# Kernel tuning notes

Measured on AMD Instinct MI355X. Metric: run time of the kernel, lower is better.

Reference implementation:

```python
import jax, jax.numpy as jnp
import numpy as np

B, S, DIM, H, HD, K, DEPTH = 2, 2048, 1024, 16, 64, 64, 8
SCALE = 1.0 / np.sqrt(HD)


def _build_cantor_routes(seq_len: int, k: int, depth: int) -> np.ndarray:
    # Vectorized version of CantorAttention._build_cantor_routes
    pos = np.arange(seq_len, dtype=np.float64)
    x = pos / max(1, seq_len - 1)
    x = np.clip(x, 1e-06, 1.0 - 1e-06)
    cantor = np.zeros(seq_len, dtype=np.float64)
    factor = 0.5
    for _ in range(depth):
        x = x * 3.0
        digit = np.floor(x)
        x = x - digit
        cantor += factor * (digit == 2.0)
        factor *= 0.5
    cantor = cantor.astype(np.float32)
    # k nearest positions in Cantor space for each position
    dist = np.abs(cantor[:, None] - cantor[None, :])  # [S, S]
    routes = np.argsort(dist, axis=1, kind='stable')[:, :k]  # [S, k]
    return routes.astype(np.int32)


def setup_inputs() -> dict:
    key = jax.random.key(0)
    k1, k2, k3, k4, k5 = jax.random.split(key, 5)
    s = 1.0 / np.sqrt(DIM)
    return {
        'x': jax.random.normal(k1, (B, S, DIM), dtype=jnp.float32),
        'w_qkv': jax.random.normal(k2, (3 * DIM, DIM), dtype=jnp.float32) * s,
        'b_qkv': jax.random.normal(k3, (3 * DIM,), dtype=jnp.float32) * 0.01,
        'w_out': jax.random.normal(k4, (DIM, DIM), dtype=jnp.float32) * s,
        'b_out': jax.random.normal(k5, (DIM,), dtype=jnp.float32) * 0.01,
        'routes': jnp.asarray(_build_cantor_routes(S, K, DEPTH)),
    }


def reference(x, w_qkv, b_qkv, w_out, b_out, routes):
    b, s, _ = x.shape
    # QKV projection (torch Linear: y = x @ W.T + b)
    qkv = x @ w_qkv.T + b_qkv                       # [B, S, 3*DIM]
    qkv = qkv.reshape(b, s, 3, H, HD).transpose(2, 0, 3, 1, 4)  # [3, B, H, S, HD]
    q, k, v = qkv[0], qkv[1], qkv[2]                # each [B, H, S, HD]
    # Gather k/v at Cantor neighbor routes: [B, H, S, K, HD]
    k_g = jnp.take(k, routes, axis=2)
    v_g = jnp.take(v, routes, axis=2)
    scores = jnp.einsum('bhqd,bhqkd->bhqk', q, k_g) * SCALE
    attn = jax.nn.softmax(scores, axis=-1)
    out = jnp.einsum('bhqk,bhqkd->bhqd', attn, v_g)  # [B, H, S, HD]
    out = out.transpose(0, 2, 1, 3).reshape(b, s, DIM)
    return out @ w_out.T + b_out
```

## Files before the change

kernel.cpp:

```cpp
#include <hip/hip_runtime.h>

#define BQ   2
#define SQ   2048
#define DIMQ 1024
#define HQ   16
#define HDQ  64
#define KQ   64
#define QKV_STRIDE (3 * DIMQ)

typedef __attribute__((ext_vector_type(8))) short short8;
typedef __attribute__((ext_vector_type(4))) float floatx4;

typedef const __attribute__((address_space(1))) unsigned short* gas_t;
typedef __attribute__((address_space(3))) unsigned short* las_t;

__device__ __forceinline__ unsigned short f2b(float f) {
    union { float f; unsigned int u; } x; x.f = f;
    unsigned int r = x.u + 0x7fffu + ((x.u >> 16) & 1u);
    return (unsigned short)(r >> 16);
}
__device__ __forceinline__ float b2f(unsigned short u) {
    union { unsigned int u; float f; } x; x.u = ((unsigned int)u) << 16;
    return x.f;
}

__global__ __launch_bounds__(256) void cast_f32_bf16(const float* __restrict__ in,
                                                     unsigned short* __restrict__ out,
                                                     int n4) {
    int i = blockIdx.x * blockDim.x + threadIdx.x;
    if (i >= n4) return;
    float4 v = ((const float4*)in)[i];
    ushort4 o;
    o.x = f2b(v.x); o.y = f2b(v.y); o.z = f2b(v.z); o.w = f2b(v.w);
    ((ushort4*)out)[i] = o;
}

template <typename CT>
__global__ __launch_bounds__(256) void gemm_bf16_nt(const unsigned short* __restrict__ A,
                                                    const unsigned short* __restrict__ B,
                                                    const float* __restrict__ bias,
                                                    CT* __restrict__ C,
                                                    int M, int N, int K) {
    __shared__ unsigned short As[128 * 32];
    __shared__ unsigned short Bs[128 * 32];

    const int tid  = threadIdx.x;
    const int lane = tid & 63;
    const int wv   = tid >> 6;
    const int wm   = (wv >> 1) * 64;
    const int wn   = (wv & 1) * 64;
    const int fr   = lane & 15;
    const int fq   = lane >> 4;

    const int m0 = blockIdx.y * 128;
    const int n0 = blockIdx.x * 128;

    floatx4 acc[4][4];
#pragma unroll
    for (int i = 0; i < 4; ++i)
#pragma unroll
        for (int j = 0; j < 4; ++j) acc[i][j] = (floatx4)(0.f);

    const unsigned short* Ab = A + (size_t)m0 * K;
    const unsigned short* Bb = B + (size_t)n0 * K;

    for (int k0 = 0; k0 < K; k0 += 32) {
#pragma unroll
        for (int iss = 0; iss < 2; ++iss) {
            const int c   = iss * 256 + wv * 64 + lane;
            const int row = c >> 2;
            const int kc  = (c & 3) << 3;
            const int ldsbase = (iss * 256 + wv * 64) * 8;
            __builtin_amdgcn_global_load_lds(
                (gas_t)(Ab + (size_t)row * K + k0 + kc), (las_t)&As[ldsbase], 16, 0, 0);
            __builtin_amdgcn_global_load_lds(
                (gas_t)(Bb + (size_t)row * K + k0 + kc), (las_t)&Bs[ldsbase], 16, 0, 0);
        }
        __syncthreads();

        short8 af[4], bf[4];
#pragma unroll
        for (int i = 0; i < 4; ++i)
            af[i] = *(const short8*)&As[(wm + i * 16 + fr) * 32 + fq * 8];
#pragma unroll
        for (int j = 0; j < 4; ++j)
            bf[j] = *(const short8*)&Bs[(wn + j * 16 + fr) * 32 + fq * 8];
#pragma unroll
        for (int i = 0; i < 4; ++i)
#pragma unroll
            for (int j = 0; j < 4; ++j)
                acc[i][j] = __builtin_amdgcn_mfma_f32_16x16x32_bf16(af[i], bf[j], acc[i][j], 0, 0, 0);
        __syncthreads();
    }

    float bv[4];
#pragma unroll
    for (int j = 0; j < 4; ++j) bv[j] = bias[n0 + wn + j * 16 + fr];
#pragma unroll
    for (int i = 0; i < 4; ++i) {
#pragma unroll
        for (int r = 0; r < 4; ++r) {
            const size_t row = (size_t)(m0 + wm + i * 16 + fq * 4 + r);
#pragma unroll
            for (int j = 0; j < 4; ++j) {
                const float v = acc[i][j][r] + bv[j];
                if constexpr (sizeof(CT) == 2)
                    C[row * N + n0 + wn + j * 16 + fr] = (CT)f2b(v);
                else
                    C[row * N + n0 + wn + j * 16 + fr] = (CT)v;
            }
        }
    }
}

__global__ __launch_bounds__(256) void attn_kernel(const unsigned short* __restrict__ qkv,
                                                   const int* __restrict__ routes,
                                                   unsigned short* __restrict__ out) {
    __shared__ float s_s[HQ][KQ + 1];
    __shared__ int   r_s[KQ];
    __shared__ float o_part[8][132];

    const int t  = threadIdx.x;
    const int id = blockIdx.x;
    const int bq = (id & 7) * 512 + (id >> 3);
    const int b  = bq >> 11;
    const int q  = bq & 2047;

    if (t < KQ) r_s[t] = routes[q * KQ + t];

    const int g    = t >> 7;
    const int th   = t & 127;
    const int h    = th >> 3;
    const int d0   = (t & 7) * 8;

    float qf[8];
    {
        const short8 q8 = *(const short8*)&qkv[((size_t)bq * 3) * DIMQ + h * HDQ + d0];
#pragma unroll
        for (int e = 0; e < 8; ++e) qf[e] = b2f((unsigned short)q8[e]);
    }
    __syncthreads();

    const size_t baseK = ((size_t)b * SQ * 3 + 1) * DIMQ + h * HDQ + d0;
    const size_t baseV = ((size_t)b * SQ * 3 + 2) * DIMQ + h * HDQ + d0;

#pragma unroll 8
    for (int jj = 0; jj < KQ / 2; ++jj) {
        const int j = jj * 2 + g;
        const int r = r_s[j];
        const short8 k8 = *(const short8*)&qkv[baseK + (size_t)r * QKV_STRIDE];
        float p = 0.f;
#pragma unroll
        for (int e = 0; e < 8; ++e) p += qf[e] * b2f((unsigned short)k8[e]);
        p += __shfl_xor(p, 1, 64);
        p += __shfl_xor(p, 2, 64);
        p += __shfl_xor(p, 4, 64);
        if ((t & 7) == 0) s_s[h][j] = p * 0.125f;
    }
    __syncthreads();

    {
        const int lane = t & 63;
        const int sh   = ((t >> 6) << 2) + (lane >> 4);
        const int i    = lane & 15;
        float v0 = s_s[sh][i], v1 = s_s[sh][i + 16], v2 = s_s[sh][i + 32], v3 = s_s[sh][i + 48];
        float mx = fmaxf(fmaxf(v0, v1), fmaxf(v2, v3));
        mx = fmaxf(mx, __shfl_xor(mx, 1, 64));
        mx = fmaxf(mx, __shfl_xor(mx, 2, 64));
        mx = fmaxf(mx, __shfl_xor(mx, 4, 64));
        mx = fmaxf(mx, __shfl_xor(mx, 8, 64));
        float e0 = __expf(v0 - mx), e1 = __expf(v1 - mx);
        float e2 = __expf(v2 - mx), e3 = __expf(v3 - mx);
        float sm = e0 + e1 + e2 + e3;
        sm += __shfl_xor(sm, 1, 64);
        sm += __shfl_xor(sm, 2, 64);
        sm += __shfl_xor(sm, 4, 64);
        sm += __shfl_xor(sm, 8, 64);
        const float inv = 1.0f / sm;
        s_s[sh][i]      = e0 * inv;
        s_s[sh][i + 16] = e1 * inv;
        s_s[sh][i + 32] = e2 * inv;
        s_s[sh][i + 48] = e3 * inv;
    }
    __syncthreads();

    float o[8];
#pragma unroll
    for (int e = 0; e < 8; ++e) o[e] = 0.f;
#pragma unroll 8
    for (int jj = 0; jj < KQ / 2; ++jj) {
        const int   j = jj * 2 + g;
        const int   r = r_s[j];
        const float w = s_s[h][j];
        const short8 v8 = *(const short8*)&qkv[baseV + (size_t)r * QKV_STRIDE];
#pragma unroll
        for (int e = 0; e < 8; ++e) o[e] += w * b2f((unsigned short)v8[e]);
    }
    if (g == 1) {
#pragma unroll
        for (int e = 0; e < 8; ++e) o_part[e][th] = o[e];
    }
    __syncthreads();
    if (g == 0) {
        ushort4 lo, hi;
        lo.x = f2b(o[0] + o_part[0][th]); lo.y = f2b(o[1] + o_part[1][th]);
        lo.z = f2b(o[2] + o_part[2][th]); lo.w = f2b(o[3] + o_part[3][th]);
        hi.x = f2b(o[4] + o_part[4][th]); hi.y = f2b(o[5] + o_part[5][th]);
        hi.z = f2b(o[6] + o_part[6][th]); hi.w = f2b(o[7] + o_part[7][th]);
        ushort4* dst = (ushort4*)&out[(size_t)bq * DIMQ + h * HDQ + d0];
        dst[0] = lo; dst[1] = hi;
    }
}

extern "C" void kernel_launch(void* const* d_in, const int* in_sizes, int n_in,
                              void* d_out, int out_size, void* d_ws, size_t ws_size,
                              hipStream_t stream) {
    const float* x      = (const float*)d_in[0];
    const float* w_qkv  = (const float*)d_in[1];
    const float* b_qkv  = (const float*)d_in[2];
    const float* w_out  = (const float*)d_in[3];
    const float* b_out  = (const float*)d_in[4];
    const int*   routes = (const int*)d_in[5];
    float* out = (float*)d_out;

    char* ws = (char*)d_ws;
    unsigned short* qkvb  = (unsigned short*)ws;
    unsigned short* xb    = (unsigned short*)(ws + 25165824);
    unsigned short* attnb = xb;
    unsigned short* wqb   = (unsigned short*)(ws + 33554432);
    unsigned short* wob   = (unsigned short*)(ws + 39845888);

    const int M = BQ * SQ;
    dim3 blk(256);

    cast_f32_bf16<<<(M * DIMQ / 4 + 255) / 256, blk, 0, stream>>>(x, xb, M * DIMQ / 4);
    cast_f32_bf16<<<(3 * DIMQ * DIMQ / 4 + 255) / 256, blk, 0, stream>>>(w_qkv, wqb, 3 * DIMQ * DIMQ / 4);
    cast_f32_bf16<<<(DIMQ * DIMQ / 4 + 255) / 256, blk, 0, stream>>>(w_out, wob, DIMQ * DIMQ / 4);

    gemm_bf16_nt<unsigned short><<<dim3(3 * DIMQ / 128, M / 128), blk, 0, stream>>>(
        xb, wqb, b_qkv, qkvb, M, 3 * DIMQ, DIMQ);

    attn_kernel<<<BQ * SQ, blk, 0, stream>>>(qkvb, routes, attnb);

    gemm_bf16_nt<float><<<dim3(DIMQ / 128, M / 128), blk, 0, stream>>>(
        attnb, wob, b_out, out, M, DIMQ, DIMQ);
}
```

Before: 207.5 us.

## Fuse casts, add online-softmax attention, and use narrower tiles for output GEMM

The three f32-to-bf16 cast launches become one kernel that dispatches on index range, removing two launches. The attention kernel now uses an online softmax. K and V gathers are issued together in a single pass, and the two half-groups' partial results are merged with max/sum rescaling. This drops the shared score buffer, two barriers and a second gather loop. The GEMM is templated on tile sizes, and the output projection uses 128x64 tiles to double its block count for better CU fill, at the cost of more extra exp work per key and less reuse per tile.

```diff
diff --git a/kernel.cpp b/kernel.cpp
--- a/kernel.cpp
+++ b/kernel.cpp
@@ -24,85 +24,94 @@
     return x.f;
 }
 
-__global__ __launch_bounds__(256) void cast_f32_bf16(const float* __restrict__ in,
-                                                     unsigned short* __restrict__ out,
-                                                     int n4) {
+__global__ __launch_bounds__(256) void cast3_f32_bf16(const float* __restrict__ s0, unsigned short* __restrict__ d0, int n0,
+                                                      const float* __restrict__ s1, unsigned short* __restrict__ d1, int n1,
+                                                      const float* __restrict__ s2, unsigned short* __restrict__ d2, int n2) {
     int i = blockIdx.x * blockDim.x + threadIdx.x;
-    if (i >= n4) return;
-    float4 v = ((const float4*)in)[i];
+    const float* s; unsigned short* d;
+    if (i < n0)                { s = s0; d = d0; }
+    else if (i < n0 + n1)      { s = s1; d = d1; i -= n0; }
+    else if (i < n0 + n1 + n2) { s = s2; d = d2; i -= n0 + n1; }
+    else return;
+    float4 v = ((const float4*)s)[i];
     ushort4 o;
     o.x = f2b(v.x); o.y = f2b(v.y); o.z = f2b(v.z); o.w = f2b(v.w);
-    ((ushort4*)out)[i] = o;
-}
-
-template <typename CT>
+    ((ushort4*)d)[i] = o;
+}
+
+template <int BM, int BN, typename CT>
 __global__ __launch_bounds__(256) void gemm_bf16_nt(const unsigned short* __restrict__ A,
                                                     const unsigned short* __restrict__ B,
                                                     const float* __restrict__ bias,
                                                     CT* __restrict__ C,
                                                     int M, int N, int K) {
-    __shared__ unsigned short As[128 * 32];
-    __shared__ unsigned short Bs[128 * 32];
+    constexpr int MI = BM / 32;
+    constexpr int NJ = BN / 32;
+    __shared__ unsigned short As[BM * 32];
+    __shared__ unsigned short Bs[BN * 32];
 
     const int tid  = threadIdx.x;
     const int lane = tid & 63;
     const int wv   = tid >> 6;
-    const int wm   = (wv >> 1) * 64;
-    const int wn   = (wv & 1) * 64;
+    const int wm   = (wv >> 1) * (BM / 2);
+    const int wn   = (wv & 1) * (BN / 2);
     const int fr   = lane & 15;
     const int fq   = lane >> 4;
 
-    const int m0 = blockIdx.y * 128;
-    const int n0 = blockIdx.x * 128;
-
-    floatx4 acc[4][4];
-#pragma unroll
-    for (int i = 0; i < 4; ++i)
-#pragma unroll
-        for (int j = 0; j < 4; ++j) acc[i][j] = (floatx4)(0.f);
+    const int m0 = blockIdx.y * BM;
+    const int n0 = blockIdx.x * BN;
+
+    floatx4 acc[MI][NJ];
+#pragma unroll
+    for (int i = 0; i < MI; ++i)
+#pragma unroll
+        for (int j = 0; j < NJ; ++j) acc[i][j] = (floatx4)(0.f);
 
     const unsigned short* Ab = A + (size_t)m0 * K;
     const unsigned short* Bb = B + (size_t)n0 * K;
 
     for (int k0 = 0; k0 < K; k0 += 32) {
 #pragma unroll
-        for (int iss = 0; iss < 2; ++iss) {
-            const int c   = iss * 256 + wv * 64 + lane;
-            const int row = c >> 2;
-            const int kc  = (c & 3) << 3;
-            const int ldsbase = (iss * 256 + wv * 64) * 8;
-            __builtin_amdgcn_global_load_lds(
-                (gas_t)(Ab + (size_t)row * K + k0 + kc), (las_t)&As[ldsbase], 16, 0, 0);
-            __builtin_amdgcn_global_load_lds(
-                (gas_t)(Bb + (size_t)row * K + k0 + kc), (las_t)&Bs[ldsbase], 16, 0, 0);
+        for (int c = 0; c < (BM + BN) * 4; c += 256) {
+            const int cc = c + tid;
+            if (cc < BM * 4) {
+                __builtin_amdgcn_global_load_lds(
+                    (gas_t)(Ab + (size_t)(cc >> 2) * K + k0 + ((cc & 3) << 3)),
+                    (las_t)&As[cc * 8], 16, 0, 0);
+            } else {
+                const int c2 = cc - BM * 4;
+                __builtin_amdgcn_global_load_lds(
+                    (gas_t)(Bb + (size_t)(c2 >> 2) * K + k0 + ((c2 & 3) << 3)),
+                    (las_t)&Bs[c2 * 8], 16, 0, 0);
+            }
         }
         __syncthreads();
 
-        short8 af[4], bf[4];
-#pragma unroll
-        for (int i = 0; i < 4; ++i)
+        short8 af[MI], bf[NJ];
+#pragma unroll
+        for (int i = 0; i < MI; ++i)
             af[i] = *(const short8*)&As[(wm + i * 16 + fr) * 32 + fq * 8];
 #pragma unroll
-        for (int j = 0; j < 4; ++j)
+        for (int j = 0; j < NJ; ++j)
             bf[j] = *(const short8*)&Bs[(wn + j * 16 + fr) * 32 + fq * 8];
 #pragma unroll
-        for (int i = 0; i < 4; ++i)
-#pragma unroll
-            for (int j = 0; j < 4; ++j)
+        for (int i = 0; i < MI; ++i)
+#pragma unroll
+            for (int j = 0; j < NJ; ++j)
                 acc[i][j] = __builtin_amdgcn_mfma_f32_16x16x32_bf16(af[i], bf[j], acc[i][j], 0, 0, 0);
         __syncthreads();
     }
 
-    float bv[4];
-#pragma unroll
-    for (int j = 0; j < 4; ++j) bv[j] = bias[n0 + wn + j * 16 + fr];
-#pragma unroll
-    for (int i = 0; i < 4; ++i) {
+    float bv[NJ];
+#pragma unroll
+    for (int j = 0; j < NJ; ++j) bv[j] = bias[n0 + wn + j * 16 + fr];
+#pragma unroll
+    for (int i = 0; i < MI; ++i) {
 #pragma unroll
         for (int r = 0; r < 4; ++r) {
             const size_t row = (size_t)(m0 + wm + i * 16 + fq * 4 + r);
 #pragma unroll
-            for (int j = 0; j < 4; ++j) {
+            for (int j = 0; j < NJ; ++j) {
                 const float v = acc[i][j][r] + bv[j];
                 if constexpr (sizeof(CT) == 2)
                     C[row * N + n0 + wn + j * 16 + fr] = (CT)f2b(v);
@@ -116,9 +125,9 @@
 __global__ __launch_bounds__(256) void attn_kernel(const unsigned short* __restrict__ qkv,
                                                    const int* __restrict__ routes,
                                                    unsigned short* __restrict__ out) {
-    __shared__ float s_s[HQ][KQ + 1];
     __shared__ int   r_s[KQ];
-    __shared__ float o_part[8][132];
+    __shared__ float m_s[128], l_s[128];
+    __shared__ float o_part[8][128];
 
     const int t  = threadIdx.x;
     const int id = blockIdx.x;
@@ -128,10 +137,10 @@
 
     if (t < KQ) r_s[t] = routes[q * KQ + t];
 
-    const int g    = t >> 7;
-    const int th   = t & 127;
-    const int h    = th >> 3;
-    const int d0   = (t & 7) * 8;
+    const int g  = t >> 7;
+    const int th = t & 127;
+    const int h  = th >> 3;
+    const int d0 = (t & 7) * 8;
 
     float qf[8];
     {
@@ -144,69 +153,51 @@
     const size_t baseK = ((size_t)b * SQ * 3 + 1) * DIMQ + h * HDQ + d0;
     const size_t baseV = ((size_t)b * SQ * 3 + 2) * DIMQ + h * HDQ + d0;
 
-#pragma unroll 8
+    float m = -1e30f, l = 0.f;
+    float o[8];
+#pragma unroll
+    for (int e = 0; e < 8; ++e) o[e] = 0.f;
+
+#pragma unroll 4
     for (int jj = 0; jj < KQ / 2; ++jj) {
         const int j = jj * 2 + g;
-        const int r = r_s[j];
-        const short8 k8 = *(const short8*)&qkv[baseK + (size_t)r * QKV_STRIDE];
+        const size_t roff = (size_t)r_s[j] * QKV_STRIDE;
+        const short8 k8 = *(const short8*)&qkv[baseK + roff];
+        const short8 v8 = *(const short8*)&qkv[baseV + roff];
         float p = 0.f;
 #pragma unroll
         for (int e = 0; e < 8; ++e) p += qf[e] * b2f((unsigned short)k8[e]);
         p += __shfl_xor(p, 1, 64);
         p += __shfl_xor(p, 2, 64);
         p += __shfl_xor(p, 4, 64);
-        if ((t & 7) == 0) s_s[h][j] = p * 0.125f;
-    }
-    __syncthreads();
-
-    {
-        const int lane = t & 63;
-        const int sh   = ((t >> 6) << 2) + (lane >> 4);
-        const int i    = lane & 15;
-        float v0 = s_s[sh][i], v1 = s_s[sh][i + 16], v2 = s_s[sh][i + 32], v3 = s_s[sh][i + 48];
-        float mx = fmaxf(fmaxf(v0, v1), fmaxf(v2, v3));
-        mx = fmaxf(mx, __shfl_xor(mx, 1, 64));
-        mx = fmaxf(mx, __shfl_xor(mx, 2, 64));
-        mx = fmaxf(mx, __shfl_xor(mx, 4, 64));
-        mx = fmaxf(mx, __shfl_xor(mx, 8, 64));
-        float e0 = __expf(v0 - mx), e1 = __expf(v1 - mx);
-        float e2 = __expf(v2 - mx), e3 = __expf(v3 - mx);
-        float sm = e0 + e1 + e2 + e3;
-        sm += __shfl_xor(sm, 1, 64);
-        sm += __shfl_xor(sm, 2, 64);
-        sm += __shfl_xor(sm, 4, 64);
-        sm += __shfl_xor(sm, 8, 64);
-        const float inv = 1.0f / sm;
-        s_s[sh][i]      = e0 * inv;
-        s_s[sh][i + 16] = e1 * inv;
-        s_s[sh][i + 32] = e2 * inv;
-        s_s[sh][i + 48] = e3 * inv;
-    }
-    __syncthreads();
-
-    float o[8];
-#pragma unroll
-    for (int e = 0; e < 8; ++e) o[e] = 0.f;
-#pragma unroll 8
-    for (int jj = 0; jj < KQ / 2; ++jj) {
-        const int   j = jj * 2 + g;
-        const int   r = r_s[j];
-        const float w = s_s[h][j];
-        const short8 v8 = *(const short8*)&qkv[baseV + (size_t)r * QKV_STRIDE];
-#pragma unroll
-        for (int e = 0; e < 8; ++e) o[e] += w * b2f((unsigned short)v8[e]);
-    }
+        const float s  = p * 0.125f;
+        const float mn = fmaxf(m, s);
+        const float al = __expf(m - mn);
+        const float pe = __expf(s - mn);
+        l = l * al + pe;
+#pragma unroll
+        for (int e = 0; e < 8; ++e) o[e] = o[e] * al + pe * b2f((unsigned short)v8[e]);
+        m = mn;
+    }
+
     if (g == 1) {
+        m_s[th] = m; l_s[th] = l;
 #pragma unroll
         for (int e = 0; e < 8; ++e) o_part[e][th] = o[e];
     }
     __syncthreads();
     if (g == 0) {
+        const float m1 = m_s[th], l1 = l_s[th];
+        const float mm = fmaxf(m, m1);
+        const float a0 = __expf(m - mm);
+        const float a1 = __expf(m1 - mm);
+        const float inv = 1.0f / (l * a0 + l1 * a1);
+        float oo[8];
+#pragma unroll
+        for (int e = 0; e < 8; ++e) oo[e] = (o[e] * a0 + o_part[e][th] * a1) * inv;
         ushort4 lo, hi;
-        lo.x = f2b(o[0] + o_part[0][th]); lo.y = f2b(o[1] + o_part[1][th]);
-        lo.z = f2b(o[2] + o_part[2][th]); lo.w = f2b(o[3] + o_part[3][th]);
-        hi.x = f2b(o[4] + o_part[4][th]); hi.y = f2b(o[5] + o_part[5][th]);
-        hi.z = f2b(o[6] + o_part[6][th]); hi.w = f2b(o[7] + o_part[7][th]);
+        lo.x = f2b(oo[0]); lo.y = f2b(oo[1]); lo.z = f2b(oo[2]); lo.w = f2b(oo[3]);
+        hi.x = f2b(oo[4]); hi.y = f2b(oo[5]); hi.z = f2b(oo[6]); hi.w = f2b(oo[7]);
         ushort4* dst = (ushort4*)&out[(size_t)bq * DIMQ + h * HDQ + d0];
         dst[0] = lo; dst[1] = hi;
     }
@@ -233,15 +224,17 @@
     const int M = BQ * SQ;
     dim3 blk(256);
 
-    cast_f32_bf16<<<(M * DIMQ / 4 + 255) / 256, blk, 0, stream>>>(x, xb, M * DIMQ / 4);
-    cast_f32_bf16<<<(3 * DIMQ * DIMQ / 4 + 255) / 256, blk, 0, stream>>>(w_qkv, wqb, 3 * DIMQ * DIMQ / 4);
-    cast_f32_bf16<<<(DIMQ * DIMQ / 4 + 255) / 256, blk, 0, stream>>>(w_out, wob, DIMQ * DIMQ / 4);
-
-    gemm_bf16_nt<unsigned short><<<dim3(3 * DIMQ / 128, M / 128), blk, 0, stream>>>(
+    {
+        const int n0 = M * DIMQ / 4, n1 = 3 * DIMQ * DIMQ / 4, n2 = DIMQ * DIMQ / 4;
+        cast3_f32_bf16<<<(n0 + n1 + n2 + 255) / 256, blk, 0, stream>>>(
+            x, xb, n0, w_qkv, wqb, n1, w_out, wob, n2);
+    }
+
+    gemm_bf16_nt<128, 128, unsigned short><<<dim3(3 * DIMQ / 128, M / 128), blk, 0, stream>>>(
         xb, wqb, b_qkv, qkvb, M, 3 * DIMQ, DIMQ);
 
     attn_kernel<<<BQ * SQ, blk, 0, stream>>>(qkvb, routes, attnb);
 
-    gemm_bf16_nt<float><<<dim3(DIMQ / 128, M / 128), blk, 0, stream>>>(
+    gemm_bf16_nt<128, 64, float><<<dim3(DIMQ / 64, M / 128), blk, 0, stream>>>(
         attnb, wob, b_out, out, M, DIMQ, DIMQ);
 }
```

New measurement: 202.3 us. 2.5% less time.
